# Kernel tuning notes

Measured on AMD Instinct MI355X. Metric: run time of the kernel, lower is better.

The kernel has to match this reference:

```python
import jax, jax.numpy as jnp
import numpy as np

N = 50000      # num nodes
E = 800000     # num edges (before self loops)
HID = 64       # hidden_channels
HEADS = 4
B = 256        # num graphs in batch
TEXT, VIS, AUD = 768, 512, 128


def setup_inputs() -> dict:
    key = jax.random.key(0)
    ks = jax.random.split(key, 24)
    rn = lambda k, shape: jax.random.normal(k, shape, dtype=jnp.float32) * 0.05
    inp = {}
    inp["x"] = jax.random.normal(ks[0], (N, TEXT), dtype=jnp.float32)
    inp["node_type"] = jax.random.randint(ks[1], (N,), 0, 3, dtype=jnp.int32)
    inp["edge_index"] = jax.random.randint(ks[2], (2, E), 0, N, dtype=jnp.int32)
    inp["batch"] = jnp.sort(jax.random.randint(ks[3], (N,), 0, B, dtype=jnp.int32))
    # modality projections
    inp["Wt"] = rn(ks[4], (TEXT, HID)); inp["bt"] = jnp.zeros((HID,), jnp.float32)
    inp["Wv"] = rn(ks[5], (VIS, HID));  inp["bv"] = jnp.zeros((HID,), jnp.float32)
    inp["Wa"] = rn(ks[6], (AUD, HID));  inp["ba"] = jnp.zeros((HID,), jnp.float32)
    # GATConv1: in=HID, out=HID, heads=HEADS, concat=True
    inp["W1"]  = rn(ks[7], (HID, HEADS * HID))
    inp["a1s"] = rn(ks[8], (HEADS, HID))
    inp["a1d"] = rn(ks[9], (HEADS, HID))
    inp["b1"]  = jnp.zeros((HEADS * HID,), jnp.float32)
    # GATConv2: in=HID*HEADS, out=HID, heads=1, concat=False
    inp["W2"]  = rn(ks[10], (HID * HEADS, HID))
    inp["a2s"] = rn(ks[11], (1, HID))
    inp["a2d"] = rn(ks[12], (1, HID))
    inp["b2"]  = jnp.zeros((HID,), jnp.float32)
    # final classifier (num_classes==2 -> out_dim 1, squeezed)
    inp["Wl"] = rn(ks[13], (HID, 1)); inp["bl"] = jnp.zeros((1,), jnp.float32)
    return inp


def gat_conv(x, edge_index, W, a_src, a_dst, bias, concat):
    """PyG-style GATConv (eval mode, add_self_loops=True, shared lin for src/dst)."""
    n = x.shape[0]
    heads, c = a_src.shape
    loops = jnp.arange(n, dtype=edge_index.dtype)
    src = jnp.concatenate([edge_index[0], loops])
    dst = jnp.concatenate([edge_index[1], loops])
    h = (x @ W).reshape(n, heads, c)                       # [N, H, C]
    alpha_s = jnp.einsum('nhc,hc->nh', h, a_src)           # [N, H]
    alpha_d = jnp.einsum('nhc,hc->nh', h, a_dst)
    e = jax.nn.leaky_relu(alpha_s[src] + alpha_d[dst], 0.2)  # [E', H]
    # numerically-stable softmax over incoming edges of each dst node
    m = jax.ops.segment_max(e, dst, num_segments=n)
    e = jnp.exp(e - m[dst])
    denom = jax.ops.segment_sum(e, dst, num_segments=n)
    alpha = e / (denom[dst] + 1e-16)                        # [E', H]
    out = jax.ops.segment_sum(h[src] * alpha[:, :, None], dst, num_segments=n)
    out = out.reshape(n, heads * c) if concat else out.mean(axis=1)
    return out + bias


def reference(x, node_type, edge_index, batch,
              Wt, bt, Wv, bv, Wa, ba,
              W1, a1s, a1d, b1, W2, a2s, a2d, b2, Wl, bl):
    # masked multimodal projection (type 0=text, 1=vision, 2=audio)
    t = x[:, :TEXT] @ Wt + bt
    v = x[:, :VIS] @ Wv + bv
    a = x[:, :AUD] @ Wa + ba
    nt = node_type[:, None]
    h = jnp.where(nt == 0, t, jnp.where(nt == 1, v, a))     # [N, HID]
    h = jax.nn.elu(gat_conv(h, edge_index, W1, a1s, a1d, b1, concat=True))
    h = gat_conv(h, edge_index, W2, a2s, a2d, b2, concat=False)  # [N, HID]
    # global mean pool over graphs
    sums = jax.ops.segment_sum(h, batch, num_segments=B)
    cnts = jax.ops.segment_sum(jnp.ones((h.shape[0], 1), h.dtype), batch, num_segments=B)
    g = sums / jnp.maximum(cnts, 1.0)                       # [B, HID]
    out = (g @ Wl + bl).squeeze(-1)                          # [B] (binary logit)
    return out
```

## Files before the change

### kernel.cpp

```cpp
#include <hip/hip_runtime.h>
#include <cstdint>
#include <cstddef>

#define TEXTD 768
#define VISD  512
#define AUDD  128

__device__ __forceinline__ float wred_sum(float v){
  #pragma unroll
  for (int m = 32; m >= 1; m >>= 1) v += __shfl_xor(v, m, 64);
  return v;
}
__device__ __forceinline__ int wred_sumi(int v){
  #pragma unroll
  for (int m = 32; m >= 1; m >>= 1) v += __shfl_xor(v, m, 64);
  return v;
}
__device__ __forceinline__ float wred_max(float v){
  #pragma unroll
  for (int m = 32; m >= 1; m >>= 1) v = fmaxf(v, __shfl_xor(v, m, 64));
  return v;
}

__global__ __launch_bounds__(256) void k_bcount(const int* __restrict__ ntype, int nN, int nblk,
                                                int* __restrict__ bcnt, int* __restrict__ deg){
  int b = blockIdx.x;
  int i = b*256 + threadIdx.x;
  int lane = threadIdx.x & 63, w = threadIdx.x >> 6;
  int ty = (i < nN) ? ntype[i] : -1;
  if (i < nN) deg[i] = 1;
  __shared__ int wc[4][3];
  #pragma unroll
  for (int t = 0; t < 3; t++){
    unsigned long long m = __ballot(ty == t);
    if (lane == 0) wc[w][t] = __popcll(m);
  }
  __syncthreads();
  if (threadIdx.x < 3){
    int t = threadIdx.x;
    bcnt[t*nblk + b] = wc[0][t] + wc[1][t] + wc[2][t] + wc[3][t];
  }
}
__global__ __launch_bounds__(1024) void k_bscan(const int* __restrict__ bcnt, int nblk, int nN,
                                                int* __restrict__ boff, int* __restrict__ toff,
                                                int* __restrict__ tcnt){
  __shared__ int s[2048];
  int n3 = nblk*3;
  int t = threadIdx.x;
  for (int i = t; i < n3; i += 1024) s[i] = bcnt[i];
  __syncthreads();
  if (t == 0){
    int run = 0;
    for (int i = 0; i < n3; i++){ int v = s[i]; s[i] = run; run += v; }
  }
  __syncthreads();
  for (int i = t; i < n3; i += 1024) boff[i] = s[i];
  if (t == 0){
    toff[0] = 0;         toff[1] = s[nblk];           toff[2] = s[2*nblk];
    tcnt[0] = s[nblk];   tcnt[1] = s[2*nblk]-s[nblk]; tcnt[2] = nN - s[2*nblk];
  }
}
__global__ __launch_bounds__(256) void k_bscatter(const int* __restrict__ ntype, int nN, int nblk,
                                                  const int* __restrict__ boff, int* __restrict__ order){
  int b = blockIdx.x;
  int i = b*256 + threadIdx.x;
  int lane = threadIdx.x & 63, w = threadIdx.x >> 6;
  int ty = (i < nN) ? ntype[i] : -1;
  __shared__ int wc[4][3];
  __shared__ int woff[4][3];
  unsigned long long masks[3];
  #pragma unroll
  for (int t = 0; t < 3; t++){
    masks[t] = __ballot(ty == t);
    if (lane == 0) wc[w][t] = __popcll(masks[t]);
  }
  __syncthreads();
  if (threadIdx.x < 3){
    int t = threadIdx.x, run = 0;
    #pragma unroll
    for (int ww = 0; ww < 4; ww++){ woff[ww][t] = run; run += wc[ww][t]; }
  }
  __syncthreads();
  if (ty >= 0){
    int r = __popcll(masks[ty] & ((1ULL << lane) - 1ULL));
    int pos = boff[ty*nblk + b] + woff[w][ty] + r;
    order[pos] = i;
  }
}

__global__ void k_deg_edges(const int* __restrict__ ei, int E, int* __restrict__ deg){
  int i = blockIdx.x*blockDim.x + threadIdx.x;
  if (i < E) atomicAdd(&deg[ei[E + i]], 1);
}
__global__ __launch_bounds__(1024) void k_sumblk(const int* __restrict__ deg, int n,
                                                 int* __restrict__ bsum){
  int b = blockIdx.x;
  int i = b*1024 + threadIdx.x;
  int lane = threadIdx.x & 63, w = threadIdx.x >> 6;
  __shared__ int wsum[16];
  int v = (i < n) ? deg[i] : 0;
  v = wred_sumi(v);
  if (lane == 0) wsum[w] = v;
  __syncthreads();
  if (threadIdx.x == 0){
    int s = 0;
    #pragma unroll
    for (int k = 0; k < 16; k++) s += wsum[k];
    bsum[b] = s;
  }
}
__global__ void k_sumscan(const int* __restrict__ bsum, int nsb, int* __restrict__ bsoff){
  if (threadIdx.x == 0){
    int run = 0;
    for (int i = 0; i < nsb; i++){ bsoff[i] = run; run += bsum[i]; }
    bsoff[nsb] = run;
  }
}
__global__ __launch_bounds__(1024) void k_offw(int* __restrict__ deg, const int* __restrict__ bsoff,
                                               int n, int* __restrict__ off){
  int b = blockIdx.x;
  int i = b*1024 + threadIdx.x;
  int t = threadIdx.x, lane = t & 63, w = t >> 6;
  __shared__ int wsum[16];
  int v = (i < n) ? deg[i] : 0;
  int orig = v;
  #pragma unroll
  for (int o = 1; o < 64; o <<= 1){ int u = __shfl_up(v, o, 64); if (lane >= o) v += u; }
  if (lane == 63) wsum[w] = v;
  __syncthreads();
  if (t < 16){
    int xv = wsum[t];
    #pragma unroll
    for (int o = 1; o < 16; o <<= 1){ int u = __shfl_up(xv, o, 16); if (t >= o) xv += u; }
    wsum[t] = xv;
  }
  __syncthreads();
  int wbase = (w == 0) ? 0 : wsum[w-1];
  int e = bsoff[b] + v + wbase - orig;
  if (i < n){ off[i] = e; deg[i] = e; }
  if (b == 0 && t == 0) off[n] = bsoff[gridDim.x];
}
__global__ void k_scatter(const int* __restrict__ ei, int E, int nN,
                          int* __restrict__ pos, int* __restrict__ csr_src){
  int i = blockIdx.x*blockDim.x + threadIdx.x;
  int total = E + nN;
  if (i >= total) return;
  int s, d;
  if (i < E){ s = ei[i]; d = ei[E + i]; } else { s = i - E; d = s; }
  int p = atomicAdd(&pos[d], 1);
  csr_src[p] = s;
}

__global__ __launch_bounds__(256) void k_afold(const float* __restrict__ W1,
    const float* __restrict__ a1s, const float* __restrict__ a1d,
    float* __restrict__ wfs, float* __restrict__ wfd){
  int t = threadIdx.x;
  int k = t & 63, h = t >> 6;
  const float* wr = W1 + (size_t)k*256 + h*64;
  const float* as = a1s + h*64;
  const float* ad = a1d + h*64;
  float s = 0.f, d = 0.f;
  for (int c = 0; c < 64; c += 4){
    float4 w  = *reinterpret_cast<const float4*>(wr + c);
    float4 sa = *reinterpret_cast<const float4*>(as + c);
    float4 da = *reinterpret_cast<const float4*>(ad + c);
    s += w.x*sa.x + w.y*sa.y + w.z*sa.z + w.w*sa.w;
    d += w.x*da.x + w.y*da.y + w.z*da.z + w.w*da.w;
  }
  wfs[k*4 + h] = s;
  wfd[k*4 + h] = d;
}

__global__ __launch_bounds__(256) void k_projgemm(const float* __restrict__ x,
    const int* __restrict__ order, const int* __restrict__ toff, const int* __restrict__ tcnt,
    const float* __restrict__ Wt, const float* __restrict__ bt,
    const float* __restrict__ Wv, const float* __restrict__ bv,
    const float* __restrict__ Wa, const float* __restrict__ ba,
    const float* __restrict__ wfs, const float* __restrict__ wfd,
    float* __restrict__ h0, float* __restrict__ as1, float* __restrict__ ad1){
  int ty = blockIdx.y;
  int cnt = tcnt[ty];
  int tile = blockIdx.x;
  if (tile*64 >= cnt) return;
  const float* W; const float* bias; int dim;
  if (ty == 0)      { W = Wt; bias = bt; dim = TEXTD; }
  else if (ty == 1) { W = Wv; bias = bv; dim = VISD; }
  else              { W = Wa; bias = ba; dim = AUDD; }
  int off = toff[ty];

  __shared__ float xsT[64][68];
  __shared__ float ws [64][68];
  __shared__ int   nid[64];

  int t = threadIdx.x;
  if (t < 64){
    int idx = tile*64 + t;
    nid[t] = (idx < cnt) ? order[off + idx] : -1;
  }
  __syncthreads();

  int node_l = t & 63;
  int ndl = nid[node_l];
  const float* xrow = x + (size_t)(ndl < 0 ? 0 : ndl) * TEXTD;
  int wrow = t >> 2, wu = t & 3;
  int wvq  = t >> 6;
  int n0 = (t & 15)*4, c0 = (t >> 4)*4, qg = t >> 4;
  float acc[4][4] = {};

  for (int k0 = 0; k0 < dim; k0 += 64){
    __syncthreads();
    #pragma unroll
    for (int j = 0; j < 4; j++){
      int f4 = wvq*4 + j;
      float4 v = *reinterpret_cast<const float4*>(xrow + k0 + f4*4);
      xsT[f4*4+0][node_l] = v.x;
      xsT[f4*4+1][node_l] = v.y;
      xsT[f4*4+2][node_l] = v.z;
      xsT[f4*4+3][node_l] = v.w;
    }
    #pragma unroll
    for (int j = 0; j < 4; j++){
      int f4 = j*4 + wu;
      float4 v = *reinterpret_cast<const float4*>(W + (size_t)(k0 + wrow)*64 + f4*4);
      *reinterpret_cast<float4*>(&ws[wrow][f4*4]) = v;
    }
    __syncthreads();
    #pragma unroll 8
    for (int kk = 0; kk < 64; kk++){
      float4 xv = *reinterpret_cast<const float4*>(&xsT[kk][n0]);
      float4 wv = *reinterpret_cast<const float4*>(&ws[kk][c0]);
      float xa[4] = {xv.x, xv.y, xv.z, xv.w};
      float wb[4] = {wv.x, wv.y, wv.z, wv.w};
      #pragma unroll
      for (int i = 0; i < 4; i++)
        #pragma unroll
        for (int j = 0; j < 4; j++)
          acc[i][j] += xa[i] * wb[j];
    }
  }

  float4 b4 = *reinterpret_cast<const float4*>(bias + c0);
  float bb[4] = {b4.x, b4.y, b4.z, b4.w};
  #pragma unroll
  for (int i = 0; i < 4; i++){
    int nd = nid[n0 + i];
    if (nd >= 0){
      float4 o4 = make_float4(acc[i][0]+bb[0], acc[i][1]+bb[1], acc[i][2]+bb[2], acc[i][3]+bb[3]);
      *reinterpret_cast<float4*>(h0 + (size_t)nd*64 + c0) = o4;
    }
  }

  __syncthreads();
  float* spart = &ws [0][0];
  float* dpart = &xsT[0][0];
  float4 wsv[4], wdv[4];
  #pragma unroll
  for (int j = 0; j < 4; j++){
    wsv[j] = *reinterpret_cast<const float4*>(wfs + (c0+j)*4);
    wdv[j] = *reinterpret_cast<const float4*>(wfd + (c0+j)*4);
  }
  #pragma unroll
  for (int i = 0; i < 4; i++){
    float hv[4];
    #pragma unroll
    for (int j = 0; j < 4; j++) hv[j] = acc[i][j] + bb[j];
    float s0v = hv[0]*wsv[0].x + hv[1]*wsv[1].x + hv[2]*wsv[2].x + hv[3]*wsv[3].x;
    float s1v = hv[0]*wsv[0].y + hv[1]*wsv[1].y + hv[2]*wsv[2].y + hv[3]*wsv[3].y;
    float s2v = hv[0]*wsv[0].z + hv[1]*wsv[1].z + hv[2]*wsv[2].z + hv[3]*wsv[3].z;
    float s3v = hv[0]*wsv[0].w + hv[1]*wsv[1].w + hv[2]*wsv[2].w + hv[3]*wsv[3].w;
    float d0v = hv[0]*wdv[0].x + hv[1]*wdv[1].x + hv[2]*wdv[2].x + hv[3]*wdv[3].x;
    float d1v = hv[0]*wdv[0].y + hv[1]*wdv[1].y + hv[2]*wdv[2].y + hv[3]*wdv[3].y;
    float d2v = hv[0]*wdv[0].z + hv[1]*wdv[1].z + hv[2]*wdv[2].z + hv[3]*wdv[3].z;
    float d3v = hv[0]*wdv[0].w + hv[1]*wdv[1].w + hv[2]*wdv[2].w + hv[3]*wdv[3].w;
    int nidx = (n0 + i)*64 + qg*4;
    spart[nidx+0]=s0v; spart[nidx+1]=s1v; spart[nidx+2]=s2v; spart[nidx+3]=s3v;
    dpart[nidx+0]=d0v; dpart[nidx+1]=d1v; dpart[nidx+2]=d2v; dpart[nidx+3]=d3v;
  }
  __syncthreads();
  if (t < 64){
    int nd = nid[t];
    if (nd >= 0){
      float s[4] = {0,0,0,0}, d[4] = {0,0,0,0};
      #pragma unroll
      for (int g = 0; g < 16; g++){
        #pragma unroll
        for (int h = 0; h < 4; h++){
          s[h] += spart[t*64 + g*4 + h];
          d[h] += dpart[t*64 + g*4 + h];
        }
      }
      *reinterpret_cast<float4*>(as1 + (size_t)nd*4) = make_float4(s[0],s[1],s[2],s[3]);
      *reinterpret_cast<float4*>(ad1 + (size_t)nd*4) = make_float4(d[0],d[1],d[2],d[3]);
    }
  }
}

__global__ __launch_bounds__(256) void k_gat1z(const int* __restrict__ off, const int* __restrict__ srcs,
    const float* __restrict__ as1, const float* __restrict__ ad1,
    const float* __restrict__ h0, float* __restrict__ z, int nN){
  int w = threadIdx.x >> 6, L = threadIdx.x & 63;
  int n = blockIdx.x*4 + w;
  __shared__ int   s_src[4][64];
  __shared__ float s_p[4][64][4];
  if (n >= nN) return;
  int hL = L >> 4, c4 = (L & 15)*4;
  float ad[4];
  { float4 a = *reinterpret_cast<const float4*>(ad1 + (size_t)n*4);
    ad[0]=a.x; ad[1]=a.y; ad[2]=a.z; ad[3]=a.w; }
  int s0 = off[n], s1 = off[n+1];
  float m[4] = {-1e30f,-1e30f,-1e30f,-1e30f};
  float den[4] = {0.f,0.f,0.f,0.f};
  float4 acc = make_float4(0.f,0.f,0.f,0.f);
  for (int base = s0; base < s1; base += 64){
    int e = base + L;
    int cl = min(64, s1 - base);
    bool valid = (e < s1);
    int sv = 0; float v[4];
    if (valid){
      sv = srcs[e];
      float4 a = *reinterpret_cast<const float4*>(as1 + (size_t)sv*4);
      float av[4] = {a.x,a.y,a.z,a.w};
      #pragma unroll
      for (int h = 0; h < 4; h++){ float tt = av[h] + ad[h]; v[h] = (tt>0.f)?tt:0.2f*tt; }
    } else {
      #pragma unroll
      for (int h = 0; h < 4; h++) v[h] = -1e30f;
    }
    float sc[4], pv[4];
    #pragma unroll
    for (int h = 0; h < 4; h++){
      float cm = wred_max(v[h]);
      float mn = fmaxf(m[h], cm);
      sc[h] = __expf(m[h] - mn);
      m[h] = mn;
      float p = valid ? __expf(v[h] - mn) : 0.f;
      den[h] = den[h]*sc[h] + wred_sum(p);
      pv[h] = p;
    }
    { float s4 = sc[hL]; acc.x*=s4; acc.y*=s4; acc.z*=s4; acc.w*=s4; }
    if (valid){
      s_src[w][L] = sv;
      *reinterpret_cast<float4*>(&s_p[w][L][0]) = make_float4(pv[0],pv[1],pv[2],pv[3]);
    }
    #pragma unroll 4
    for (int e2 = 0; e2 < cl; e2++){
      int sr = s_src[w][e2];
      float pp = s_p[w][e2][hL];
      float4 hv = *reinterpret_cast<const float4*>(h0 + (size_t)sr*64 + c4);
      acc.x += pp*hv.x; acc.y += pp*hv.y; acc.z += pp*hv.z; acc.w += pp*hv.w;
    }
  }
  float dl = den[hL] + 1e-16f;
  *reinterpret_cast<float4*>(z + (size_t)n*256 + hL*64 + c4) =
      make_float4(acc.x/dl, acc.y/dl, acc.z/dl, acc.w/dl);
}

__global__ __launch_bounds__(256) void k_fuse12(const float* __restrict__ z,
    const float* __restrict__ W1, const float* __restrict__ b1,
    const float* __restrict__ W2, const float* __restrict__ a2s, const float* __restrict__ a2d,
    float* __restrict__ h2, float* __restrict__ as2, float* __restrict__ ad2, int nN){
  int base = blockIdx.x*64;
  __shared__ float xsT[64][68];
  __shared__ float ws [64][68];
  __shared__ float sPart[16][64];
  __shared__ float dPart[16][64];

  int t = threadIdx.x;
  int row = t >> 2, fq = t & 3;
  int ndl = base + row; if (ndl >= nN) ndl = nN - 1;
  int n0 = (t & 15)*4, c0 = (t >> 4)*4, qg = t >> 4;
  float h2acc[4][4] = {};

  for (int q = 0; q < 4; q++){
    __syncthreads();
    {
      const float* zr = z + (size_t)ndl*256 + q*64;
      #pragma unroll
      for (int j = 0; j < 4; j++){
        int f4 = j*4 + fq;
        float4 v = *reinterpret_cast<const float4*>(zr + f4*4);
        xsT[f4*4+0][row] = v.x; xsT[f4*4+1][row] = v.y;
        xsT[f4*4+2][row] = v.z; xsT[f4*4+3][row] = v.w;
      }
    }
    #pragma unroll
    for (int j = 0; j < 4; j++){
      int f4 = j*4 + fq;
      float4 v = *reinterpret_cast<const float4*>(W1 + (size_t)row*256 + q*64 + f4*4);
      *reinterpret_cast<float4*>(&ws[row][f4*4]) = v;
    }
    __syncthreads();
    float racc[4][4] = {};
    #pragma unroll 8
    for (int k = 0; k < 64; k++){
      float4 xv = *reinterpret_cast<const float4*>(&xsT[k][n0]);
      float4 wv = *reinterpret_cast<const float4*>(&ws[k][c0]);
      float xa[4] = {xv.x, xv.y, xv.z, xv.w};
      float wb[4] = {wv.x, wv.y, wv.z, wv.w};
      #pragma unroll
      for (int i = 0; i < 4; i++)
        #pragma unroll
        for (int j = 0; j < 4; j++)
          racc[i][j] += xa[i] * wb[j];
    }
    {
      float4 b4 = *reinterpret_cast<const float4*>(b1 + q*64 + c0);
      float bb[4] = {b4.x, b4.y, b4.z, b4.w};
      #pragma unroll
      for (int i = 0; i < 4; i++)
        #pragma unroll
        for (int j = 0; j < 4; j++){
          float u = racc[i][j] + bb[j];
          racc[i][j] = (u > 0.f) ? u : expm1f(u);
        }
    }
    __syncthreads();
    #pragma unroll
    for (int i = 0; i < 4; i++)
      #pragma unroll
      for (int j = 0; j < 4; j++)
        xsT[c0+j][n0+i] = racc[i][j];
    #pragma unroll
    for (int j = 0; j < 4; j++){
      int f4 = j*4 + fq;
      float4 v = *reinterpret_cast<const float4*>(W2 + (size_t)(q*64 + row)*64 + f4*4);
      *reinterpret_cast<float4*>(&ws[row][f4*4]) = v;
    }
    __syncthreads();
    #pragma unroll 8
    for (int k = 0; k < 64; k++){
      float4 xv = *reinterpret_cast<const float4*>(&xsT[k][n0]);
      float4 wv = *reinterpret_cast<const float4*>(&ws[k][c0]);
      float xa[4] = {xv.x, xv.y, xv.z, xv.w};
      float wb[4] = {wv.x, wv.y, wv.z, wv.w};
      #pragma unroll
      for (int i = 0; i < 4; i++)
        #pragma unroll
        for (int j = 0; j < 4; j++)
          h2acc[i][j] += xa[i] * wb[j];
    }
  }

  float avs[4], avd[4];
  {
    float4 s4 = *reinterpret_cast<const float4*>(a2s + c0);
    float4 d4 = *reinterpret_cast<const float4*>(a2d + c0);
    avs[0]=s4.x; avs[1]=s4.y; avs[2]=s4.z; avs[3]=s4.w;
    avd[0]=d4.x; avd[1]=d4.y; avd[2]=d4.z; avd[3]=d4.w;
  }
  #pragma unroll
  for (int i = 0; i < 4; i++){
    int nd = base + n0 + i;
    float sp = h2acc[i][0]*avs[0] + h2acc[i][1]*avs[1] + h2acc[i][2]*avs[2] + h2acc[i][3]*avs[3];
    float dp = h2acc[i][0]*avd[0] + h2acc[i][1]*avd[1] + h2acc[i][2]*avd[2] + h2acc[i][3]*avd[3];
    sPart[qg][n0+i] = sp;
    dPart[qg][n0+i] = dp;
    if (nd < nN){
      float4 o4 = make_float4(h2acc[i][0], h2acc[i][1], h2acc[i][2], h2acc[i][3]);
      *reinterpret_cast<float4*>(h2 + (size_t)nd*64 + c0) = o4;
    }
  }
  __syncthreads();
  if (t < 64){
    int nd = base + t;
    if (nd < nN){
      float s = 0.f, d = 0.f;
      #pragma unroll
      for (int g = 0; g < 16; g++){ s += sPart[g][t]; d += dPart[g][t]; }
      as2[nd] = s;
      ad2[nd] = d;
    }
  }
}

__global__ __launch_bounds__(256) void k_gat2v(const int* __restrict__ off, const int* __restrict__ srcs,
    const float* __restrict__ as2, const float* __restrict__ ad2,
    const float* __restrict__ h2, const float* __restrict__ b2,
    float* __restrict__ g2, int nN){
  int w = threadIdx.x >> 6, L = threadIdx.x & 63;
  int n = blockIdx.x*4 + w;
  if (n >= nN) return;
  int g = L >> 4, c4 = (L & 15)*4;
  float ad = ad2[n];
  int s0 = off[n], s1 = off[n+1];
  float m = -1e30f, den = 0.f;
  float4 acc = make_float4(0.f,0.f,0.f,0.f);
  for (int base = s0; base < s1; base += 64){
    int e = base + L;
    int cl = min(64, s1 - base);
    bool valid = (e < s1);
    int sv = 0; float v = -1e30f;
    if (valid){
      sv = srcs[e];
      float tt = as2[sv] + ad;
      v = (tt>0.f)?tt:0.2f*tt;
    }
    float cm = wred_max(v);
    float mn = fmaxf(m, cm);
    float sc = __expf(m - mn);
    m = mn;
    float p = valid ? __expf(v - mn) : 0.f;
    den = den*sc + wred_sum(p);
    acc.x*=sc; acc.y*=sc; acc.z*=sc; acc.w*=sc;
    int iters = (cl + 3) >> 2;
    for (int it = 0; it < iters; ++it){
      int e2   = it*4 + g;
      int esrc = (e2 < cl) ? e2 : (cl - 1);
      int   sr = __shfl(sv, esrc, 64);
      float pp = __shfl(p,  esrc, 64);
      if (e2 < cl){
        float4 hv = *reinterpret_cast<const float4*>(h2 + (size_t)sr*64 + c4);
        acc.x += pp*hv.x; acc.y += pp*hv.y; acc.z += pp*hv.z; acc.w += pp*hv.w;
      }
    }
  }
  #pragma unroll
  for (int s = 16; s <= 32; s <<= 1){
    acc.x += __shfl_xor(acc.x, s, 64);
    acc.y += __shfl_xor(acc.y, s, 64);
    acc.z += __shfl_xor(acc.z, s, 64);
    acc.w += __shfl_xor(acc.w, s, 64);
  }
  float dl = den + 1e-16f;
  if (L < 16){
    float4 b4 = *reinterpret_cast<const float4*>(b2 + c4);
    float4 o4 = make_float4(acc.x/dl + b4.x, acc.y/dl + b4.y,
                            acc.z/dl + b4.z, acc.w/dl + b4.w);
    *reinterpret_cast<float4*>(g2 + (size_t)n*64 + c4) = o4;
  }
}

__global__ void k_bstart(const int* __restrict__ batch, int nN, int B, int* __restrict__ bstart){
  int i = blockIdx.x*blockDim.x + threadIdx.x;
  if (i < nN){
    int prev = (i == 0) ? -1 : batch[i-1];
    int cur  = batch[i];
    for (int b = prev+1; b <= cur; b++) bstart[b] = i;
  } else if (i == nN){
    int last = batch[nN-1];
    for (int b = last+1; b <= B; b++) bstart[b] = nN;
  }
}

__global__ __launch_bounds__(64) void k_pool(const float* __restrict__ g2, const int* __restrict__ bstart,
    const float* __restrict__ Wl, const float* __restrict__ bl, float* __restrict__ out, int B){
  int b = blockIdx.x, c = threadIdx.x;
  int r0 = bstart[b], r1 = bstart[b+1];
  float s = 0.f;
  int i = r0;
  for (; i + 4 <= r1; i += 4){
    s += g2[(size_t)(i+0)*64 + c];
    s += g2[(size_t)(i+1)*64 + c];
    s += g2[(size_t)(i+2)*64 + c];
    s += g2[(size_t)(i+3)*64 + c];
  }
  for (; i < r1; i++) s += g2[(size_t)i*64 + c];
  float g = s / fmaxf((float)(r1 - r0), 1.f);
  float v = wred_sum(g * Wl[c]);
  if (c == 0) out[b] = v + bl[0];
}

extern "C" void kernel_launch(void* const* d_in, const int* in_sizes, int n_in,
                              void* d_out, int out_size, void* d_ws, size_t ws_size,
                              hipStream_t stream){
  const float* x    = (const float*)d_in[0];
  const int*   ntyp = (const int*)  d_in[1];
  const int*   ei   = (const int*)  d_in[2];
  const int*   batch= (const int*)  d_in[3];
  const float* Wt = (const float*)d_in[4];
  const float* bt = (const float*)d_in[5];
  const float* Wv = (const float*)d_in[6];
  const float* bv = (const float*)d_in[7];
  const float* Wa = (const float*)d_in[8];
  const float* ba = (const float*)d_in[9];
  const float* W1 = (const float*)d_in[10];
  const float* a1s= (const float*)d_in[11];
  const float* a1d= (const float*)d_in[12];
  const float* b1 = (const float*)d_in[13];
  const float* W2 = (const float*)d_in[14];
  const float* a2s= (const float*)d_in[15];
  const float* a2d= (const float*)d_in[16];
  const float* b2 = (const float*)d_in[17];
  const float* Wl = (const float*)d_in[18];
  const float* bl = (const float*)d_in[19];

  const int N = in_sizes[1];
  const int E = in_sizes[2] / 2;
  const int B = out_size;
  const int nblk = (N + 255)/256;
  const int nsb  = (N + 1023)/1024;

  char* ws = (char*)d_ws;
  size_t o = 0;
  auto alloc = [&](size_t bytes) -> void* {
    void* p = ws + o;
    o = (o + bytes + 255) & ~(size_t)255;
    return p;
  };
  int*   csr_off = (int*)  alloc((size_t)(N+1)*4);
  int*   pos     = (int*)  alloc((size_t)N*4);
  int*   csr_src = (int*)  alloc((size_t)(E+N)*4);
  float* as1     = (float*)alloc((size_t)N*4*4);
  float* ad1     = (float*)alloc((size_t)N*4*4);
  float* h0      = (float*)alloc((size_t)N*64*4);
  float* zbuf    = (float*)alloc((size_t)N*256*4);
  int*   bstart  = (int*)  alloc((size_t)(B+1)*4);
  int*   bcnt    = (int*)  alloc((size_t)nblk*3*4);
  int*   boff    = (int*)  alloc((size_t)nblk*3*4);
  int*   toff    = (int*)  alloc(3*4);
  int*   tcnt    = (int*)  alloc(3*4);
  int*   order   = (int*)  alloc((size_t)N*4);
  float* wfs     = (float*)alloc(256*4);
  float* wfd     = (float*)alloc(256*4);
  int*   bsum    = (int*)  alloc((size_t)nsb*4);
  int*   bsoff   = (int*)  alloc((size_t)(nsb+1)*4);
  float* h2  = h0;
  float* as2 = as1;
  float* ad2 = ad1;
  float* g2  = zbuf;

  k_bcount  <<<nblk, 256, 0, stream>>>(ntyp, N, nblk, bcnt, pos);
  k_bscan   <<<1, 1024, 0, stream>>>(bcnt, nblk, N, boff, toff, tcnt);
  k_bscatter<<<nblk, 256, 0, stream>>>(ntyp, N, nblk, boff, order);

  k_deg_edges<<<(E + 255)/256, 256, 0, stream>>>(ei, E, pos);
  k_sumblk  <<<nsb, 1024, 0, stream>>>(pos, N, bsum);
  k_sumscan <<<1, 64, 0, stream>>>(bsum, nsb, bsoff);
  k_offw    <<<nsb, 1024, 0, stream>>>(pos, bsoff, N, csr_off);
  k_scatter <<<(E + N + 255)/256, 256, 0, stream>>>(ei, E, N, pos, csr_src);

  k_bstart<<<(N + 1 + 255)/256, 256, 0, stream>>>(batch, N, B, bstart);

  k_afold<<<1, 256, 0, stream>>>(W1, a1s, a1d, wfs, wfd);

  {
    dim3 g((N + 63)/64, 3);
    k_projgemm<<<g, 256, 0, stream>>>(x, order, toff, tcnt, Wt, bt, Wv, bv, Wa, ba,
                                      wfs, wfd, h0, as1, ad1);
  }

  k_gat1z <<<(N + 3)/4, 256, 0, stream>>>(csr_off, csr_src, as1, ad1, h0, zbuf, N);
  k_fuse12<<<(N + 63)/64, 256, 0, stream>>>(zbuf, W1, b1, W2, a2s, a2d, h2, as2, ad2, N);

  k_gat2v<<<(N + 3)/4, 256, 0, stream>>>(csr_off, csr_src, as2, ad2, h2, b2, g2, N);
  k_pool<<<B, 64, 0, stream>>>(g2, bstart, Wl, bl, (float*)d_out, B);
}
```

Baseline: 350.1 us.

## Fuse front-end preprocessing kernels and enlarge projection GEMM tile to 128 nodes

Merges the node-type count, degree atomics and batch-start kernels into one launch, and folds the attention-vector precompute into the scan kernel. The degree buffer is now zeroed by a memset, and the self-loop +1 is added during the scans. Separately, the projection GEMM now handles 128 nodes per block with an 8x4 register tile to raise reuse of the weight tile, and splits the src/dst attention partials into two passes through one shared buffer. This trades fewer launches and more per-thread work for higher register pressure and extra barriers.

```diff
diff --git a/kernel.cpp b/kernel.cpp
--- a/kernel.cpp
+++ b/kernel.cpp
@@ -22,31 +22,60 @@
   return v;
 }
 
-__global__ __launch_bounds__(256) void k_bcount(const int* __restrict__ ntype, int nN, int nblk,
-                                                int* __restrict__ bcnt, int* __restrict__ deg){
+__global__ __launch_bounds__(256) void k_front(const int* __restrict__ ntype,
+    const int* __restrict__ batch, const int* __restrict__ ei,
+    int nN, int E, int B, int nblk,
+    int* __restrict__ bcnt, int* __restrict__ deg, int* __restrict__ bstart){
   int b = blockIdx.x;
-  int i = b*256 + threadIdx.x;
-  int lane = threadIdx.x & 63, w = threadIdx.x >> 6;
-  int ty = (i < nN) ? ntype[i] : -1;
-  if (i < nN) deg[i] = 1;
+  int t = threadIdx.x;
+  int i = b*256 + t;
+  int lane = t & 63, w = t >> 6;
+  int ty = (b < nblk && i < nN) ? ntype[i] : -1;
   __shared__ int wc[4][3];
   #pragma unroll
-  for (int t = 0; t < 3; t++){
-    unsigned long long m = __ballot(ty == t);
-    if (lane == 0) wc[w][t] = __popcll(m);
-  }
-  __syncthreads();
-  if (threadIdx.x < 3){
-    int t = threadIdx.x;
-    bcnt[t*nblk + b] = wc[0][t] + wc[1][t] + wc[2][t] + wc[3][t];
-  }
-}
-__global__ __launch_bounds__(1024) void k_bscan(const int* __restrict__ bcnt, int nblk, int nN,
-                                                int* __restrict__ boff, int* __restrict__ toff,
-                                                int* __restrict__ tcnt){
+  for (int h = 0; h < 3; h++){
+    unsigned long long m = __ballot(ty == h);
+    if (lane == 0) wc[w][h] = __popcll(m);
+  }
+  __syncthreads();
+  if (b < nblk && t < 3){
+    int h = t;
+    bcnt[h*nblk + b] = wc[0][h] + wc[1][h] + wc[2][h] + wc[3][h];
+  }
+  if (i < nN){
+    int prev = (i == 0) ? -1 : batch[i-1];
+    int cur  = batch[i];
+    for (int bb = prev+1; bb <= cur; bb++) bstart[bb] = i;
+  } else if (i == nN){
+    int last = batch[nN-1];
+    for (int bb = last+1; bb <= B; bb++) bstart[bb] = nN;
+  }
+  if (i < E) atomicAdd(&deg[ei[E + i]], 1);
+}
+
+__global__ __launch_bounds__(1024) void k_bscan_afold(const int* __restrict__ bcnt, int nblk, int nN,
+    int* __restrict__ boff, int* __restrict__ toff, int* __restrict__ tcnt,
+    const float* __restrict__ W1, const float* __restrict__ a1s, const float* __restrict__ a1d,
+    float* __restrict__ wfs, float* __restrict__ wfd){
+  int t = threadIdx.x;
+  if (t < 256){
+    int k = t & 63, h = t >> 6;
+    const float* wr = W1 + (size_t)k*256 + h*64;
+    const float* as = a1s + h*64;
+    const float* ad = a1d + h*64;
+    float s = 0.f, d = 0.f;
+    for (int c = 0; c < 64; c += 4){
+      float4 wv = *reinterpret_cast<const float4*>(wr + c);
+      float4 sa = *reinterpret_cast<const float4*>(as + c);
+      float4 da = *reinterpret_cast<const float4*>(ad + c);
+      s += wv.x*sa.x + wv.y*sa.y + wv.z*sa.z + wv.w*sa.w;
+      d += wv.x*da.x + wv.y*da.y + wv.z*da.z + wv.w*da.w;
+    }
+    wfs[k*4 + h] = s;
+    wfd[k*4 + h] = d;
+  }
   __shared__ int s[2048];
   int n3 = nblk*3;
-  int t = threadIdx.x;
   for (int i = t; i < n3; i += 1024) s[i] = bcnt[i];
   __syncthreads();
   if (t == 0){
@@ -60,6 +89,7 @@
     tcnt[0] = s[nblk];   tcnt[1] = s[2*nblk]-s[nblk]; tcnt[2] = nN - s[2*nblk];
   }
 }
+
 __global__ __launch_bounds__(256) void k_bscatter(const int* __restrict__ ntype, int nN, int nblk,
                                                   const int* __restrict__ boff, int* __restrict__ order){
   int b = blockIdx.x;
@@ -88,17 +118,13 @@
   }
 }
 
-__global__ void k_deg_edges(const int* __restrict__ ei, int E, int* __restrict__ deg){
-  int i = blockIdx.x*blockDim.x + threadIdx.x;
-  if (i < E) atomicAdd(&deg[ei[E + i]], 1);
-}
 __global__ __launch_bounds__(1024) void k_sumblk(const int* __restrict__ deg, int n,
                                                  int* __restrict__ bsum){
   int b = blockIdx.x;
   int i = b*1024 + threadIdx.x;
   int lane = threadIdx.x & 63, w = threadIdx.x >> 6;
   __shared__ int wsum[16];
-  int v = (i < n) ? deg[i] : 0;
+  int v = (i < n) ? deg[i] + 1 : 0;
   v = wred_sumi(v);
   if (lane == 0) wsum[w] = v;
   __syncthreads();
@@ -122,7 +148,7 @@
   int i = b*1024 + threadIdx.x;
   int t = threadIdx.x, lane = t & 63, w = t >> 6;
   __shared__ int wsum[16];
-  int v = (i < n) ? deg[i] : 0;
+  int v = (i < n) ? deg[i] + 1 : 0;
   int orig = v;
   #pragma unroll
   for (int o = 1; o < 64; o <<= 1){ int u = __shfl_up(v, o, 64); if (lane >= o) v += u; }
@@ -149,26 +175,6 @@
   if (i < E){ s = ei[i]; d = ei[E + i]; } else { s = i - E; d = s; }
   int p = atomicAdd(&pos[d], 1);
   csr_src[p] = s;
-}
-
-__global__ __launch_bounds__(256) void k_afold(const float* __restrict__ W1,
-    const float* __restrict__ a1s, const float* __restrict__ a1d,
-    float* __restrict__ wfs, float* __restrict__ wfd){
-  int t = threadIdx.x;
-  int k = t & 63, h = t >> 6;
-  const float* wr = W1 + (size_t)k*256 + h*64;
-  const float* as = a1s + h*64;
-  const float* ad = a1d + h*64;
-  float s = 0.f, d = 0.f;
-  for (int c = 0; c < 64; c += 4){
-    float4 w  = *reinterpret_cast<const float4*>(wr + c);
-    float4 sa = *reinterpret_cast<const float4*>(as + c);
-    float4 da = *reinterpret_cast<const float4*>(ad + c);
-    s += w.x*sa.x + w.y*sa.y + w.z*sa.z + w.w*sa.w;
-    d += w.x*da.x + w.y*da.y + w.z*da.z + w.w*da.w;
-  }
-  wfs[k*4 + h] = s;
-  wfd[k*4 + h] = d;
 }
 
 __global__ __launch_bounds__(256) void k_projgemm(const float* __restrict__ x,
@@ -181,42 +187,40 @@
   int ty = blockIdx.y;
   int cnt = tcnt[ty];
   int tile = blockIdx.x;
-  if (tile*64 >= cnt) return;
+  if (tile*128 >= cnt) return;
   const float* W; const float* bias; int dim;
   if (ty == 0)      { W = Wt; bias = bt; dim = TEXTD; }
   else if (ty == 1) { W = Wv; bias = bv; dim = VISD; }
   else              { W = Wa; bias = ba; dim = AUDD; }
   int off = toff[ty];
 
-  __shared__ float xsT[64][68];
+  __shared__ float xsT[64][136];
   __shared__ float ws [64][68];
-  __shared__ int   nid[64];
+  __shared__ int   nid[128];
 
   int t = threadIdx.x;
-  if (t < 64){
-    int idx = tile*64 + t;
+  if (t < 128){
+    int idx = tile*128 + t;
     nid[t] = (idx < cnt) ? order[off + idx] : -1;
   }
   __syncthreads();
 
-  int node_l = t & 63;
-  int ndl = nid[node_l];
-  const float* xrow = x + (size_t)(ndl < 0 ? 0 : ndl) * TEXTD;
+  int row = t >> 1, half = t & 1;
+  int ndr = nid[row];
+  const float* xrow = x + (size_t)(ndr < 0 ? 0 : ndr) * TEXTD;
   int wrow = t >> 2, wu = t & 3;
-  int wvq  = t >> 6;
-  int n0 = (t & 15)*4, c0 = (t >> 4)*4, qg = t >> 4;
-  float acc[4][4] = {};
+  int ng = t & 15, cg = t >> 4;
+  int n0 = ng*8, c0 = cg*4;
+  float acc[8][4] = {};
 
   for (int k0 = 0; k0 < dim; k0 += 64){
     __syncthreads();
     #pragma unroll
-    for (int j = 0; j < 4; j++){
-      int f4 = wvq*4 + j;
+    for (int j = 0; j < 8; j++){
+      int f4 = half*8 + j;
       float4 v = *reinterpret_cast<const float4*>(xrow + k0 + f4*4);
-      xsT[f4*4+0][node_l] = v.x;
-      xsT[f4*4+1][node_l] = v.y;
-      xsT[f4*4+2][node_l] = v.z;
-      xsT[f4*4+3][node_l] = v.w;
+      xsT[f4*4+0][row] = v.x; xsT[f4*4+1][row] = v.y;
+      xsT[f4*4+2][row] = v.z; xsT[f4*4+3][row] = v.w;
     }
     #pragma unroll
     for (int j = 0; j < 4; j++){
@@ -225,14 +229,15 @@
       *reinterpret_cast<float4*>(&ws[wrow][f4*4]) = v;
     }
     __syncthreads();
-    #pragma unroll 8
+    #pragma unroll 4
     for (int kk = 0; kk < 64; kk++){
-      float4 xv = *reinterpret_cast<const float4*>(&xsT[kk][n0]);
+      float4 x0 = *reinterpret_cast<const float4*>(&xsT[kk][n0]);
+      float4 x1 = *reinterpret_cast<const float4*>(&xsT[kk][n0+4]);
       float4 wv = *reinterpret_cast<const float4*>(&ws[kk][c0]);
-      float xa[4] = {xv.x, xv.y, xv.z, xv.w};
-      float wb[4] = {wv.x, wv.y, wv.z, wv.w};
-      #pragma unroll
-      for (int i = 0; i < 4; i++)
+      float xa[8] = {x0.x,x0.y,x0.z,x0.w, x1.x,x1.y,x1.z,x1.w};
+      float wb[4] = {wv.x,wv.y,wv.z,wv.w};
+      #pragma unroll
+      for (int i = 0; i < 8; i++)
         #pragma unroll
         for (int j = 0; j < 4; j++)
           acc[i][j] += xa[i] * wb[j];
@@ -242,7 +247,7 @@
   float4 b4 = *reinterpret_cast<const float4*>(bias + c0);
   float bb[4] = {b4.x, b4.y, b4.z, b4.w};
   #pragma unroll
-  for (int i = 0; i < 4; i++){
+  for (int i = 0; i < 8; i++){
     int nd = nid[n0 + i];
     if (nd >= 0){
       float4 o4 = make_float4(acc[i][0]+bb[0], acc[i][1]+bb[1], acc[i][2]+bb[2], acc[i][3]+bb[3]);
@@ -250,46 +255,58 @@
     }
   }
 
-  __syncthreads();
-  float* spart = &ws [0][0];
-  float* dpart = &xsT[0][0];
+  float* part = &xsT[0][0];
   float4 wsv[4], wdv[4];
   #pragma unroll
   for (int j = 0; j < 4; j++){
     wsv[j] = *reinterpret_cast<const float4*>(wfs + (c0+j)*4);
     wdv[j] = *reinterpret_cast<const float4*>(wfd + (c0+j)*4);
   }
-  #pragma unroll
-  for (int i = 0; i < 4; i++){
+  __syncthreads();
+  #pragma unroll
+  for (int i = 0; i < 8; i++){
     float hv[4];
     #pragma unroll
     for (int j = 0; j < 4; j++) hv[j] = acc[i][j] + bb[j];
-    float s0v = hv[0]*wsv[0].x + hv[1]*wsv[1].x + hv[2]*wsv[2].x + hv[3]*wsv[3].x;
-    float s1v = hv[0]*wsv[0].y + hv[1]*wsv[1].y + hv[2]*wsv[2].y + hv[3]*wsv[3].y;
-    float s2v = hv[0]*wsv[0].z + hv[1]*wsv[1].z + hv[2]*wsv[2].z + hv[3]*wsv[3].z;
-    float s3v = hv[0]*wsv[0].w + hv[1]*wsv[1].w + hv[2]*wsv[2].w + hv[3]*wsv[3].w;
-    float d0v = hv[0]*wdv[0].x + hv[1]*wdv[1].x + hv[2]*wdv[2].x + hv[3]*wdv[3].x;
-    float d1v = hv[0]*wdv[0].y + hv[1]*wdv[1].y + hv[2]*wdv[2].y + hv[3]*wdv[3].y;
-    float d2v = hv[0]*wdv[0].z + hv[1]*wdv[1].z + hv[2]*wdv[2].z + hv[3]*wdv[3].z;
-    float d3v = hv[0]*wdv[0].w + hv[1]*wdv[1].w + hv[2]*wdv[2].w + hv[3]*wdv[3].w;
-    int nidx = (n0 + i)*64 + qg*4;
-    spart[nidx+0]=s0v; spart[nidx+1]=s1v; spart[nidx+2]=s2v; spart[nidx+3]=s3v;
-    dpart[nidx+0]=d0v; dpart[nidx+1]=d1v; dpart[nidx+2]=d2v; dpart[nidx+3]=d3v;
-  }
-  __syncthreads();
-  if (t < 64){
+    int nidx = (n0 + i)*64 + cg*4;
+    part[nidx+0] = hv[0]*wsv[0].x + hv[1]*wsv[1].x + hv[2]*wsv[2].x + hv[3]*wsv[3].x;
+    part[nidx+1] = hv[0]*wsv[0].y + hv[1]*wsv[1].y + hv[2]*wsv[2].y + hv[3]*wsv[3].y;
+    part[nidx+2] = hv[0]*wsv[0].z + hv[1]*wsv[1].z + hv[2]*wsv[2].z + hv[3]*wsv[3].z;
+    part[nidx+3] = hv[0]*wsv[0].w + hv[1]*wsv[1].w + hv[2]*wsv[2].w + hv[3]*wsv[3].w;
+  }
+  __syncthreads();
+  if (t < 128){
     int nd = nid[t];
     if (nd >= 0){
-      float s[4] = {0,0,0,0}, d[4] = {0,0,0,0};
-      #pragma unroll
-      for (int g = 0; g < 16; g++){
+      float s[4] = {0,0,0,0};
+      #pragma unroll
+      for (int g = 0; g < 16; g++)
         #pragma unroll
-        for (int h = 0; h < 4; h++){
-          s[h] += spart[t*64 + g*4 + h];
-          d[h] += dpart[t*64 + g*4 + h];
-        }
-      }
+        for (int h = 0; h < 4; h++) s[h] += part[t*64 + g*4 + h];
       *reinterpret_cast<float4*>(as1 + (size_t)nd*4) = make_float4(s[0],s[1],s[2],s[3]);
+    }
+  }
+  __syncthreads();
+  #pragma unroll
+  for (int i = 0; i < 8; i++){
+    float hv[4];
+    #pragma unroll
+    for (int j = 0; j < 4; j++) hv[j] = acc[i][j] + bb[j];
+    int nidx = (n0 + i)*64 + cg*4;
+    part[nidx+0] = hv[0]*wdv[0].x + hv[1]*wdv[1].x + hv[2]*wdv[2].x + hv[3]*wdv[3].x;
+    part[nidx+1] = hv[0]*wdv[0].y + hv[1]*wdv[1].y + hv[2]*wdv[2].y + hv[3]*wdv[3].y;
+    part[nidx+2] = hv[0]*wdv[0].z + hv[1]*wdv[1].z + hv[2]*wdv[2].z + hv[3]*wdv[3].z;
+    part[nidx+3] = hv[0]*wdv[0].w + hv[1]*wdv[1].w + hv[2]*wdv[2].w + hv[3]*wdv[3].w;
+  }
+  __syncthreads();
+  if (t < 128){
+    int nd = nid[t];
+    if (nd >= 0){
+      float d[4] = {0,0,0,0};
+      #pragma unroll
+      for (int g = 0; g < 16; g++)
+        #pragma unroll
+        for (int h = 0; h < 4; h++) d[h] += part[t*64 + g*4 + h];
       *reinterpret_cast<float4*>(ad1 + (size_t)nd*4) = make_float4(d[0],d[1],d[2],d[3]);
     }
   }
@@ -527,18 +544,6 @@
     float4 o4 = make_float4(acc.x/dl + b4.x, acc.y/dl + b4.y,
                             acc.z/dl + b4.z, acc.w/dl + b4.w);
     *reinterpret_cast<float4*>(g2 + (size_t)n*64 + c4) = o4;
-  }
-}
-
-__global__ void k_bstart(const int* __restrict__ batch, int nN, int B, int* __restrict__ bstart){
-  int i = blockIdx.x*blockDim.x + threadIdx.x;
-  if (i < nN){
-    int prev = (i == 0) ? -1 : batch[i-1];
-    int cur  = batch[i];
-    for (int b = prev+1; b <= cur; b++) bstart[b] = i;
-  } else if (i == nN){
-    int last = batch[nN-1];
-    for (int b = last+1; b <= B; b++) bstart[b] = nN;
   }
 }
 
@@ -619,22 +624,19 @@
   float* ad2 = ad1;
   float* g2  = zbuf;
 
-  k_bcount  <<<nblk, 256, 0, stream>>>(ntyp, N, nblk, bcnt, pos);
-  k_bscan   <<<1, 1024, 0, stream>>>(bcnt, nblk, N, boff, toff, tcnt);
+  hipMemsetAsync(pos, 0, (size_t)N*4, stream);
+
+  k_front<<<(E + 255)/256, 256, 0, stream>>>(ntyp, batch, ei, N, E, B, nblk, bcnt, pos, bstart);
+  k_bscan_afold<<<1, 1024, 0, stream>>>(bcnt, nblk, N, boff, toff, tcnt, W1, a1s, a1d, wfs, wfd);
   k_bscatter<<<nblk, 256, 0, stream>>>(ntyp, N, nblk, boff, order);
 
-  k_deg_edges<<<(E + 255)/256, 256, 0, stream>>>(ei, E, pos);
   k_sumblk  <<<nsb, 1024, 0, stream>>>(pos, N, bsum);
   k_sumscan <<<1, 64, 0, stream>>>(bsum, nsb, bsoff);
   k_offw    <<<nsb, 1024, 0, stream>>>(pos, bsoff, N, csr_off);
   k_scatter <<<(E + N + 255)/256, 256, 0, stream>>>(ei, E, N, pos, csr_src);
 
-  k_bstart<<<(N + 1 + 255)/256, 256, 0, stream>>>(batch, N, B, bstart);
-
-  k_afold<<<1, 256, 0, stream>>>(W1, a1s, a1d, wfs, wfd);
-
   {
-    dim3 g((N + 63)/64, 3);
+    dim3 g((N + 127)/128, 3);
     k_projgemm<<<g, 256, 0, stream>>>(x, order, toff, tcnt, Wt, bt, Wv, bv, Wa, ba,
                                       wfs, wfd, h0, as1, ad1);
   }
```

New measurement: 374.3 us. 6.9% more time.
